# Kernel optimization log

Measured on AMD Instinct MI355X. Metric: run time of the kernel, lower is better.

The kernel has to match this reference:

```python
import jax, jax.numpy as jnp
import numpy as np

ALPHA = 1.0

def setup_inputs() -> dict:
    key = jax.random.key(0)
    k1, k2 = jax.random.split(key)
    B, T, F = 8, 4096, 1024
    x = jax.random.normal(k1, (B, T, F), dtype=jnp.float32)
    # ragged valid lengths in [T//2, T]; mask[b, t] = t < length[b]
    lengths = jax.random.randint(k2, (B,), T // 2, T + 1)
    attention_mask = (jnp.arange(T)[None, :] < lengths[:, None]).astype(jnp.int32)
    return {"input_values": x, "attention_mask": attention_mask}


def reference(input_values, attention_mask):
    # input_values: [B,T,F]; attention_mask: [B,T] (1 for valid, 0 for pad)
    m = attention_mask.astype(input_values.dtype)[..., None]          # [B,T,1]
    L = jnp.sum(m, axis=1)                                            # [B,1]
    # k: per-channel mean over valid timesteps (torch mean over dims [-1,-2])
    k = jnp.sum(input_values * m, axis=1) / L                         # [B,F]
    k_centered = k - jnp.mean(k, axis=-1, keepdims=True)              # [B,F] (center over channels)
    kd = jnp.sqrt(jnp.sum(k_centered ** 2, axis=-1, keepdims=True))   # [B,1]
    # center each timestep over channels
    x_centered = input_values - jnp.mean(input_values, axis=-1, keepdims=True)  # [B,T,F]
    qd = jnp.sqrt(jnp.sum(x_centered ** 2, axis=-1))                  # [B,T]
    num = jnp.einsum('btf,bf->bt', x_centered, k_centered)            # [B,T]
    C_qk = num / (qd * kd)                                            # [B,T]
    A = (1.0 - jax.nn.sigmoid(C_qk)) ** ALPHA                         # [B,T]
    # apply attention and zero out padded positions (original zero-pads)
    out = input_values * A[..., None] * m                             # [B,T,F]
    return out
```

## Files before the change

kernel.cpp:

```cpp
#include <hip/hip_runtime.h>
#include <math.h>

#define BB 8
#define TT 4096
#define FF 1024
#define F4 (FF / 4)
#define TS 256
#define TCHUNK (TT / TS)

typedef float vfloat4 __attribute__((ext_vector_type(4)));

__global__ __launch_bounds__(256) void k1_partial(const float4* __restrict__ x4,
                                                  const int* __restrict__ mask,
                                                  float4* __restrict__ part4,
                                                  float* __restrict__ Sk,
                                                  float* __restrict__ Skk) {
    const int ts  = blockIdx.x;
    const int b   = blockIdx.y;
    const int tid = threadIdx.x;

    if (ts == 0 && tid == 0) { Sk[b] = 0.f; Skk[b] = 0.f; }

    const int4* mrow = (const int4*)(mask + (size_t)b * TT + ts * TCHUNK);
    int4 m0 = mrow[0], m1 = mrow[1], m2 = mrow[2], m3 = mrow[3];
    const int nv = m0.x + m0.y + m0.z + m0.w + m1.x + m1.y + m1.z + m1.w
                 + m2.x + m2.y + m2.z + m2.w + m3.x + m3.y + m3.z + m3.w;
    if (nv == 0) return;

    const float4* xb = x4 + ((size_t)b * TT + (size_t)ts * TCHUNK) * F4 + tid;
    float4 acc = make_float4(0.f, 0.f, 0.f, 0.f);
    #pragma unroll 8
    for (int t = 0; t < nv; ++t) {
        float4 v = xb[(size_t)t * F4];
        acc.x += v.x; acc.y += v.y; acc.z += v.z; acc.w += v.w;
    }
    part4[((size_t)b * TS + ts) * F4 + tid] = acc;
}

__global__ __launch_bounds__(256) void k2_stats(const float* __restrict__ part,
                                                const int* __restrict__ mask,
                                                float* __restrict__ kbuf,
                                                float* __restrict__ Sk,
                                                float* __restrict__ Skk) {
    __shared__ float red[8][32];
    __shared__ float Lred[4];

    const int tid   = threadIdx.x;
    const int wave  = tid >> 6;
    const int lane  = tid & 63;
    const int b2    = blockIdx.x >> 5;
    const int fbase = (blockIdx.x & 31) * 32;

    int c = 0;
    #pragma unroll
    for (int i = 0; i < 16; ++i) c += mask[(size_t)b2 * TT + tid + 256 * i];
    float fc = (float)c;
    #pragma unroll
    for (int off = 32; off; off >>= 1) fc += __shfl_xor(fc, off);
    if (lane == 0) Lred[wave] = fc;
    __syncthreads();
    const float Lf  = Lred[0] + Lred[1] + Lred[2] + Lred[3];
    const int   nts = ((int)Lf + TCHUNK - 1) / TCHUNK;

    const int f     = fbase + (tid & 31);
    const int slice = tid >> 5;
    float s = 0.f;
    for (int t = slice; t < nts; t += 8)
        s += part[((size_t)b2 * TS + t) * FF + f];
    red[slice][tid & 31] = s;
    __syncthreads();

    if (tid < 32) {
        float sum = 0.f;
        #pragma unroll
        for (int sl = 0; sl < 8; ++sl) sum += red[sl][tid];
        const float kv = sum / Lf;
        kbuf[(size_t)b2 * FF + fbase + tid] = kv;
        float a = kv, q = kv * kv;
        #pragma unroll
        for (int off = 16; off; off >>= 1) {
            a += __shfl_xor(a, off);
            q += __shfl_xor(q, off);
        }
        if (tid == 0) {
            atomicAdd(&Sk[b2],  a);
            atomicAdd(&Skk[b2], q);
        }
    }
}

__global__ __launch_bounds__(256) void k3_apply(const float4* __restrict__ x4,
                                                const int* __restrict__ mask,
                                                const float4* __restrict__ kb4,
                                                const float* __restrict__ Sk,
                                                const float* __restrict__ Skk,
                                                float4* __restrict__ out4) {
    const int wave = threadIdx.x >> 6;
    const int lane = threadIdx.x & 63;
    const int b    = blockIdx.y;
    const int rowbase = blockIdx.x * 16 + wave * 4;
    const size_t base = ((size_t)b * TT + rowbase) * F4;

    const int4 m4 = *(const int4*)(mask + (size_t)b * TT + rowbase);
    const int  nv = m4.x + m4.y + m4.z + m4.w;

    for (int i = nv; i < 4; ++i) {
        vfloat4* orow = (vfloat4*)(out4 + base + (size_t)i * F4);
        vfloat4 z = (vfloat4)(0.f);
        #pragma unroll
        for (int j = 0; j < 4; ++j)
            __builtin_nontemporal_store(z, orow + lane + 64 * j);
    }
    if (nv == 0) return;

    const float4* krow = kb4 + (size_t)b * F4;
    float4 kv[4];
    #pragma unroll
    for (int j = 0; j < 4; ++j) kv[j] = krow[lane + 64 * j];

    const float sk  = Sk[b];
    const float kd  = sqrtf(fmaxf(Skk[b] - sk * sk * (1.0f / FF), 0.f));

    float4 xn[4];
    #pragma unroll
    for (int j = 0; j < 4; ++j) xn[j] = (x4 + base)[lane + 64 * j];

    for (int i = 0; i < nv; ++i) {
        float4 xv[4];
        #pragma unroll
        for (int j = 0; j < 4; ++j) xv[j] = xn[j];
        if (i + 1 < nv) {
            const float4* xrow = x4 + base + (size_t)(i + 1) * F4;
            #pragma unroll
            for (int j = 0; j < 4; ++j) xn[j] = xrow[lane + 64 * j];
        }

        float s1 = 0.f, s2 = 0.f, s3 = 0.f;
        #pragma unroll
        for (int j = 0; j < 4; ++j) {
            s1 += xv[j].x + xv[j].y + xv[j].z + xv[j].w;
            s2 = fmaf(xv[j].x, xv[j].x, fmaf(xv[j].y, xv[j].y,
                 fmaf(xv[j].z, xv[j].z, fmaf(xv[j].w, xv[j].w, s2))));
            s3 = fmaf(xv[j].x, kv[j].x, fmaf(xv[j].y, kv[j].y,
                 fmaf(xv[j].z, kv[j].z, fmaf(xv[j].w, kv[j].w, s3))));
        }
        #pragma unroll
        for (int off = 32; off; off >>= 1) {
            s1 += __shfl_xor(s1, off);
            s2 += __shfl_xor(s2, off);
            s3 += __shfl_xor(s3, off);
        }

        const float mx  = s1 * (1.0f / FF);
        const float num = s3 - mx * sk;
        const float qd  = sqrtf(fmaxf(s2 - s1 * s1 * (1.0f / FF), 0.f));
        const float C   = num / (qd * kd);
        const float A   = 1.0f / (1.0f + __expf(C));

        vfloat4* orow = (vfloat4*)(out4 + base + (size_t)i * F4);
        #pragma unroll
        for (int j = 0; j < 4; ++j) {
            vfloat4 o;
            o.x = xv[j].x * A; o.y = xv[j].y * A;
            o.z = xv[j].z * A; o.w = xv[j].w * A;
            __builtin_nontemporal_store(o, orow + lane + 64 * j);
        }
    }
}

extern "C" void kernel_launch(void* const* d_in, const int* in_sizes, int n_in,
                              void* d_out, int out_size, void* d_ws, size_t ws_size,
                              hipStream_t stream) {
    const float* x    = (const float*)d_in[0];
    const int*   mask = (const int*)d_in[1];
    float*       out  = (float*)d_out;

    float* part = (float*)d_ws;
    float* kbuf = part + (size_t)BB * TS * FF;
    float* Sk   = kbuf + (size_t)BB * FF;
    float* Skk  = Sk + BB;

    k1_partial<<<dim3(TS, BB), 256, 0, stream>>>((const float4*)x, mask,
                                                 (float4*)part, Sk, Skk);
    k2_stats<<<256, 256, 0, stream>>>(part, mask, kbuf, Sk, Skk);
    k3_apply<<<dim3(TT / 16, BB), 256, 0, stream>>>((const float4*)x, mask,
                                                    (const float4*)kbuf, Sk, Skk,
                                                    (float4*)out);
}
```

Baseline: 252.0 us.

## Fuse partial-sum and stats kernels via last-block-done atomic counter

Merges the column-sum and statistics kernels into one. The last block per batch, found through an atomic ready counter and threadfence, reduces the partials and writes k, Sk and Skk directly instead of accumulating them with atomics. The time chunk count is halved, so each block sums 32 rows and there are fewer partials to reduce. This removes one kernel launch and its dependency gap, but adds a memset launch. It also leaves the final reduction to a single serial block per batch, with fewer blocks in the first pass.

```diff
diff --git a/kernel.cpp b/kernel.cpp
--- a/kernel.cpp
+++ b/kernel.cpp
@@ -5,91 +5,87 @@
 #define TT 4096
 #define FF 1024
 #define F4 (FF / 4)
-#define TS 256
+#define TS 128
 #define TCHUNK (TT / TS)
 
 typedef float vfloat4 __attribute__((ext_vector_type(4)));
 
-__global__ __launch_bounds__(256) void k1_partial(const float4* __restrict__ x4,
-                                                  const int* __restrict__ mask,
-                                                  float4* __restrict__ part4,
-                                                  float* __restrict__ Sk,
-                                                  float* __restrict__ Skk) {
-    const int ts  = blockIdx.x;
-    const int b   = blockIdx.y;
-    const int tid = threadIdx.x;
+__global__ __launch_bounds__(256) void kA_sum_stats(const float4* __restrict__ x4,
+                                                    const int* __restrict__ mask,
+                                                    float4* __restrict__ part4,
+                                                    float4* __restrict__ kbuf4,
+                                                    float* __restrict__ Sk,
+                                                    float* __restrict__ Skk,
+                                                    int* __restrict__ ready) {
+    const int ts   = blockIdx.x;
+    const int b    = blockIdx.y;
+    const int tid  = threadIdx.x;
+    const int wave = tid >> 6;
+    const int lane = tid & 63;
 
-    if (ts == 0 && tid == 0) { Sk[b] = 0.f; Skk[b] = 0.f; }
+    const int* mrow = mask + (size_t)b * TT + ts * TCHUNK;
+    int nv = 0;
+    #pragma unroll
+    for (int i = 0; i < TCHUNK; ++i) nv += mrow[i];
 
-    const int4* mrow = (const int4*)(mask + (size_t)b * TT + ts * TCHUNK);
-    int4 m0 = mrow[0], m1 = mrow[1], m2 = mrow[2], m3 = mrow[3];
-    const int nv = m0.x + m0.y + m0.z + m0.w + m1.x + m1.y + m1.z + m1.w
-                 + m2.x + m2.y + m2.z + m2.w + m3.x + m3.y + m3.z + m3.w;
-    if (nv == 0) return;
+    if (nv > 0) {
+        const float4* xb = x4 + ((size_t)b * TT + (size_t)ts * TCHUNK) * F4 + tid;
+        float4 acc = make_float4(0.f, 0.f, 0.f, 0.f);
+        #pragma unroll 8
+        for (int t = 0; t < nv; ++t) {
+            float4 v = xb[(size_t)t * F4];
+            acc.x += v.x; acc.y += v.y; acc.z += v.z; acc.w += v.w;
+        }
+        part4[((size_t)b * TS + ts) * F4 + tid] = acc;
+    }
 
-    const float4* xb = x4 + ((size_t)b * TT + (size_t)ts * TCHUNK) * F4 + tid;
-    float4 acc = make_float4(0.f, 0.f, 0.f, 0.f);
-    #pragma unroll 8
-    for (int t = 0; t < nv; ++t) {
-        float4 v = xb[(size_t)t * F4];
-        acc.x += v.x; acc.y += v.y; acc.z += v.z; acc.w += v.w;
-    }
-    part4[((size_t)b * TS + ts) * F4 + tid] = acc;
-}
-
-__global__ __launch_bounds__(256) void k2_stats(const float* __restrict__ part,
-                                                const int* __restrict__ mask,
-                                                float* __restrict__ kbuf,
-                                                float* __restrict__ Sk,
-                                                float* __restrict__ Skk) {
-    __shared__ float red[8][32];
-    __shared__ float Lred[4];
-
-    const int tid   = threadIdx.x;
-    const int wave  = tid >> 6;
-    const int lane  = tid & 63;
-    const int b2    = blockIdx.x >> 5;
-    const int fbase = (blockIdx.x & 31) * 32;
+    __threadfence();
+    __shared__ int last;
+    if (tid == 0) last = (atomicAdd(&ready[b], 1) == TS - 1);
+    __syncthreads();
+    if (!last) return;
+    __threadfence();
 
     int c = 0;
     #pragma unroll
-    for (int i = 0; i < 16; ++i) c += mask[(size_t)b2 * TT + tid + 256 * i];
+    for (int i = 0; i < 16; ++i) c += mask[(size_t)b * TT + tid + 256 * i];
     float fc = (float)c;
     #pragma unroll
     for (int off = 32; off; off >>= 1) fc += __shfl_xor(fc, off);
+    __shared__ float Lred[4];
     if (lane == 0) Lred[wave] = fc;
     __syncthreads();
     const float Lf  = Lred[0] + Lred[1] + Lred[2] + Lred[3];
     const int   nts = ((int)Lf + TCHUNK - 1) / TCHUNK;
 
-    const int f     = fbase + (tid & 31);
-    const int slice = tid >> 5;
-    float s = 0.f;
-    for (int t = slice; t < nts; t += 8)
-        s += part[((size_t)b2 * TS + t) * FF + f];
-    red[slice][tid & 31] = s;
+    float4 s = make_float4(0.f, 0.f, 0.f, 0.f);
+    #pragma unroll 4
+    for (int t = 0; t < nts; ++t) {
+        float4 v = part4[((size_t)b * TS + t) * F4 + tid];
+        s.x += v.x; s.y += v.y; s.z += v.z; s.w += v.w;
+    }
+    const float invL = 1.0f / Lf;
+    float4 kv;
+    kv.x = s.x * invL; kv.y = s.y * invL; kv.z = s.z * invL; kv.w = s.w * invL;
+    kbuf4[(size_t)b * F4 + tid] = kv;
+
+    float a = kv.x + kv.y + kv.z + kv.w;
+    float q = kv.x * kv.x + kv.y * kv.y + kv.z * kv.z + kv.w * kv.w;
+    #pragma unroll
+    for (int off = 32; off; off >>= 1) {
+        a += __shfl_xor(a, off);
+        q += __shfl_xor(q, off);
+    }
+    __shared__ float Ared[4], Qred[4];
+    if (lane == 0) { Ared[wave] = a; Qred[wave] = q; }
     __syncthreads();
-
-    if (tid < 32) {
-        float sum = 0.f;
-        #pragma unroll
-        for (int sl = 0; sl < 8; ++sl) sum += red[sl][tid];
-        const float kv = sum / Lf;
-        kbuf[(size_t)b2 * FF + fbase + tid] = kv;
-        float a = kv, q = kv * kv;
-        #pragma unroll
-        for (int off = 16; off; off >>= 1) {
-            a += __shfl_xor(a, off);
-            q += __shfl_xor(q, off);
-        }
-        if (tid == 0) {
-            atomicAdd(&Sk[b2],  a);
-            atomicAdd(&Skk[b2], q);
-        }
+    if (tid == 0) {
+        Sk[b]  = Ared[0] + Ared[1] + Ared[2] + Ared[3];
+        Skk[b] = Qred[0] + Qred[1] + Qred[2] + Qred[3];
     }
 }
 
-__global__ __launch_bounds__(256) void k3_apply(const float4* __restrict__ x4,
+__global__ __launch_bounds__(256) void kB_apply(const float4* __restrict__ x4,
                                                 const int* __restrict__ mask,
                                                 const float4* __restrict__ kb4,
                                                 const float* __restrict__ Sk,
@@ -118,8 +114,8 @@
     #pragma unroll
     for (int j = 0; j < 4; ++j) kv[j] = krow[lane + 64 * j];
 
-    const float sk  = Sk[b];
-    const float kd  = sqrtf(fmaxf(Skk[b] - sk * sk * (1.0f / FF), 0.f));
+    const float sk = Sk[b];
+    const float kd = sqrtf(fmaxf(Skk[b] - sk * sk * (1.0f / FF), 0.f));
 
     float4 xn[4];
     #pragma unroll
@@ -175,15 +171,18 @@
     const int*   mask = (const int*)d_in[1];
     float*       out  = (float*)d_out;
 
-    float* part = (float*)d_ws;
-    float* kbuf = part + (size_t)BB * TS * FF;
-    float* Sk   = kbuf + (size_t)BB * FF;
-    float* Skk  = Sk + BB;
+    float* part  = (float*)d_ws;
+    float* kbuf  = part + (size_t)BB * TS * FF;
+    float* Sk    = kbuf + (size_t)BB * FF;
+    float* Skk   = Sk + BB;
+    int*   ready = (int*)(Skk + BB);
 
-    k1_partial<<<dim3(TS, BB), 256, 0, stream>>>((const float4*)x, mask,
-                                                 (float4*)part, Sk, Skk);
-    k2_stats<<<256, 256, 0, stream>>>(part, mask, kbuf, Sk, Skk);
-    k3_apply<<<dim3(TT / 16, BB), 256, 0, stream>>>((const float4*)x, mask,
+    hipMemsetAsync(ready, 0, BB * sizeof(int), stream);
+
+    kA_sum_stats<<<dim3(TS, BB), 256, 0, stream>>>((const float4*)x, mask,
+                                                   (float4*)part, (float4*)kbuf,
+                                                   Sk, Skk, ready);
+    kB_apply<<<dim3(TT / 16, BB), 256, 0, stream>>>((const float4*)x, mask,
                                                     (const float4*)kbuf, Sk, Skk,
                                                     (float4*)out);
 }
```

After: 418.3 us. 66.0% more time.
